# Kernel optimization log

Measured on AMD Instinct MI355X. Metric: run time of the kernel, lower is better.

## Reference

```python
import jax, jax.numpy as jnp
import numpy as np

B, S, D = 4, 2048, 1024
H = 16
HD = D // H  # head_dim = 64


def setup_inputs() -> dict:
    key = jax.random.key(0)
    ks = jax.random.split(key, 8)
    scale = 1.0 / np.sqrt(D)
    return {
        "X_Q": jax.random.normal(ks[0], (B, S, D), dtype=jnp.float32),
        "X_KV": jax.random.normal(ks[1], (B, S, D), dtype=jnp.float32),
        # q_proj: Linear(D, D), weights stored as (in, out)
        "q_w": jax.random.normal(ks[2], (D, D), dtype=jnp.float32) * scale,
        "q_b": jax.random.normal(ks[3], (D,), dtype=jnp.float32) * scale,
        # kv_proj: Linear(D, 2*D)
        "kv_w": jax.random.normal(ks[4], (D, 2 * D), dtype=jnp.float32) * scale,
        "kv_b": jax.random.normal(ks[5], (2 * D,), dtype=jnp.float32) * scale,
        # out_proj: Linear(D, D) (query_dim == input_dim)
        "out_w": jax.random.normal(ks[6], (D, D), dtype=jnp.float32) * scale,
        "out_b": jax.random.normal(ks[7], (D,), dtype=jnp.float32) * scale,
    }


def reference(X_Q, X_KV, q_w, q_b, kv_w, kv_b, out_w, out_b):
    # projections
    q = X_Q @ q_w + q_b                      # [b, s, D]
    kv = X_KV @ kv_w + kv_b                  # [b, l, 2D]
    k, v = jnp.split(kv, 2, axis=-1)         # each [b, l, D]

    def split_heads(t):
        b, m, _ = t.shape
        return t.reshape(b, m, H, HD).transpose(0, 2, 1, 3)  # [b, h, m, d]

    q, k, v = split_heads(q), split_heads(k), split_heads(v)

    # standard attention: full SxL scores (non-flash path)
    scores = jnp.einsum("bhsd,bhld->bhsl", q, k) / np.sqrt(HD)
    attn = jax.nn.softmax(scores, axis=-1)   # dropout_p = 0 -> identity
    out = jnp.einsum("bhsl,bhld->bhsd", attn, v)

    # merge heads: [b, h, s, d] -> [b, s, h*d]
    out = out.transpose(0, 2, 1, 3).reshape(B, S, D)
    return out @ out_w + out_b
```

## Files before the change

kernel.cpp:

```cpp
#include <hip/hip_runtime.h>
#include <hip/hip_bf16.h>
#include <math.h>

#define B_  4
#define S_  2048
#define D_  1024
#define H_  16
#define HD_ 64

typedef __bf16 bf16;
typedef __bf16 bf16x4 __attribute__((ext_vector_type(4)));
typedef __bf16 bf16x8 __attribute__((ext_vector_type(8)));
typedef float  floatx4 __attribute__((ext_vector_type(4)));
typedef unsigned short ushort8 __attribute__((ext_vector_type(8)));

#define QSCALE 0.18033688011112042f

__device__ __forceinline__ void async_load16(const bf16* g, bf16* l) {
  __builtin_amdgcn_global_load_lds(
      (const __attribute__((address_space(1))) void*)g,
      (__attribute__((address_space(3))) void*)l, 16, 0, 0);
}

__global__ __launch_bounds__(256) void cast_both(
    const float* __restrict__ ina, bf16* __restrict__ outa,
    const float* __restrict__ inb, bf16* __restrict__ outb) {
  int bid = blockIdx.x;
  const float* in;
  bf16* out;
  int i;
  if (bid < 8192) { in = ina; out = outa; i = (bid * 256 + threadIdx.x) * 4; }
  else            { in = inb; out = outb; i = ((bid - 8192) * 256 + threadIdx.x) * 4; }
  float4 v = *reinterpret_cast<const float4*>(in + i);
  bf16x4 o;
  o[0] = (bf16)v.x; o[1] = (bf16)v.y; o[2] = (bf16)v.z; o[3] = (bf16)v.w;
  *reinterpret_cast<bf16x4*>(out + i) = o;
}

__global__ __launch_bounds__(256) void transcast_all(
    const float* __restrict__ qw, bf16* __restrict__ qwT,
    const float* __restrict__ kvw, bf16* __restrict__ kvwT,
    const float* __restrict__ ow, bf16* __restrict__ owT) {
  __shared__ float tile[32][33];
  int bid = blockIdx.x;
  const float* in; bf16* out; int N, lb;
  if (bid < 1024)      { in = qw;  out = qwT;  N = 1024; lb = bid; }
  else if (bid < 3072) { in = kvw; out = kvwT; N = 2048; lb = bid - 1024; }
  else                 { in = ow;  out = owT;  N = 1024; lb = bid - 3072; }
  int nx = N >> 5;
  int n0 = (lb % nx) * 32, k0 = (lb / nx) * 32;
  int tx = threadIdx.x & 31, ty = threadIdx.x >> 5;
  #pragma unroll
  for (int i = ty; i < 32; i += 8)
    tile[i][tx] = in[(size_t)(k0 + i) * N + n0 + tx];
  __syncthreads();
  #pragma unroll
  for (int i = ty; i < 32; i += 8)
    out[(size_t)(n0 + i) * 1024 + k0 + tx] = (bf16)tile[tx][i];
}

template <int MODE>
__global__ __launch_bounds__(256) void gemm_bt(
    const bf16* __restrict__ A, const bf16* __restrict__ Bt,
    const float* __restrict__ bias, void* __restrict__ out,
    int M, int N, int K) {
  __shared__ bf16 As[128][64];
  __shared__ bf16 Bs[128][64];

  const int tid  = threadIdx.x;
  const int m0   = blockIdx.y * 128;
  const int n0   = blockIdx.x * 128;
  const int w    = tid >> 6;
  const int lane = tid & 63;
  const int lr   = lane & 15;
  const int lq   = lane >> 4;
  const int wm   = (w >> 1) * 64;
  const int wn   = (w & 1) * 64;

  const int srow = lane >> 3;
  const int sg   = (lane & 7) ^ srow;
  const bf16* aptr = A  + (size_t)(m0 + 32 * w + srow) * K + 8 * sg;
  const bf16* bptr = Bt + (size_t)(n0 + 32 * w + srow) * K + 8 * sg;

  floatx4 acc[4][4];
  #pragma unroll
  for (int i = 0; i < 4; i++)
    #pragma unroll
    for (int j = 0; j < 4; j++)
      acc[i][j] = floatx4{0.f, 0.f, 0.f, 0.f};

  for (int k0 = 0; k0 < K; k0 += 64) {
    __syncthreads();
    #pragma unroll
    for (int p = 0; p < 4; p++) {
      async_load16(aptr + (size_t)8 * p * K + k0, &As[32 * w + 8 * p][0]);
      async_load16(bptr + (size_t)8 * p * K + k0, &Bs[32 * w + 8 * p][0]);
    }
    __syncthreads();
    #pragma unroll
    for (int kc = 0; kc < 2; kc++) {
      const int sw = 8 * ((kc * 4 + lq) ^ (lr & 7));
      bf16x8 af[4], bfv[4];
      #pragma unroll
      for (int t = 0; t < 4; t++)
        af[t] = *reinterpret_cast<const bf16x8*>(&As[wm + 16 * t + lr][sw]);
      #pragma unroll
      for (int t = 0; t < 4; t++)
        bfv[t] = *reinterpret_cast<const bf16x8*>(&Bs[wn + 16 * t + lr][sw]);
      #pragma unroll
      for (int i = 0; i < 4; i++)
        #pragma unroll
        for (int j = 0; j < 4; j++)
          acc[i][j] = __builtin_amdgcn_mfma_f32_16x16x32_bf16(af[i], bfv[j], acc[i][j], 0, 0, 0);
    }
  }

  #pragma unroll
  for (int i = 0; i < 4; i++) {
    int row_base = m0 + wm + 16 * i + lq * 4;
    #pragma unroll
    for (int j = 0; j < 4; j++) {
      int col = n0 + wn + 16 * j + lr;
      float bv = bias[col];
      if (MODE == 2 && col >= 1024) {
        int b = row_base >> 11, s0 = row_base & 2047;
        int c = col - 1024, h = c >> 6, d = c & 63;
        bf16* Vt = (bf16*)out + (size_t)B_ * H_ * S_ * HD_;
        bf16x4 pk;
        #pragma unroll
        for (int r = 0; r < 4; r++) pk[r] = (bf16)(acc[i][j][r] + bv);
        *reinterpret_cast<bf16x4*>(
            &Vt[(((size_t)b * H_ + h) * HD_ + d) * S_ + s0]) = pk;
        continue;
      }
      #pragma unroll
      for (int r = 0; r < 4; r++) {
        int row = row_base + r;
        float v = acc[i][j][r] + bv;
        if (MODE == 0) {
          ((float*)out)[(size_t)row * N + col] = v;
        } else if (MODE == 1) {
          int b = row >> 11, s = row & 2047;
          int h = col >> 6, d = col & 63;
          ((bf16*)out)[(((size_t)b * H_ + h) * S_ + s) * HD_ + d] =
              (bf16)(v * QSCALE);
        } else {
          int b = row >> 11, s = row & 2047;
          int h = col >> 6, d = col & 63;
          ((bf16*)out)[(((size_t)b * H_ + h) * S_ + s) * HD_ + d] = (bf16)v;
        }
      }
    }
  }
}

__global__ __launch_bounds__(256, 2) void attn_kernel(
    const bf16* __restrict__ Q, const bf16* __restrict__ Kb,
    const bf16* __restrict__ Vt, bf16* __restrict__ out) {
  __shared__ bf16 smem[32768];

  const int tid  = threadIdx.x;
  const int w    = tid >> 6;
  const int lane = tid & 63;
  const int lr   = lane & 15;
  const int lq   = lane >> 4;
  const int q0   = blockIdx.x * 256;
  const int bh   = blockIdx.y;
  const size_t base = (size_t)bh * S_ * HD_;

  bf16* pw = smem + 16384 + w * 4096;

  const int srow = lane >> 3;
  const int sg   = (lane & 7) ^ srow;

  const bf16* kptr = Kb + base + (size_t)(16 * w + srow) * HD_ + 8 * sg;
  const bf16* vptr = Vt + base + (size_t)(16 * w + srow) * S_  + 8 * sg;

  #pragma unroll
  for (int p = 0; p < 2; p++) {
    async_load16(kptr + (size_t)8 * p * HD_, smem + (16 * w + 8 * p) * 64);
    async_load16(vptr + (size_t)8 * p * S_,  smem + 4096 + (16 * w + 8 * p) * 64);
  }

  bf16x8 bq[4][2];
  #pragma unroll
  for (int g = 0; g < 4; g++) {
    const bf16* qrow = Q + base + (size_t)(q0 + 64 * w + 16 * g + lr) * HD_;
    bq[g][0] = *reinterpret_cast<const bf16x8*>(qrow + lq * 8);
    bq[g][1] = *reinterpret_cast<const bf16x8*>(qrow + 32 + lq * 8);
  }

  const int sw0 = 8 * ((0 + lq) ^ (lr & 7));
  const int sw1 = 8 * ((4 + lq) ^ (lr & 7));
  const int pcolbase = 4 * (lq & 1);
  const int pswz = lr & 7;

  float l_i[4] = {0.f, 0.f, 0.f, 0.f};
  floatx4 o_acc[4][4];
  #pragma unroll
  for (int g = 0; g < 4; g++)
    #pragma unroll
    for (int t = 0; t < 4; t++) o_acc[g][t] = floatx4{0.f, 0.f, 0.f, 0.f};

  __syncthreads();

  const int NIT = S_ / 64;
  for (int it = 0; it < NIT; it++) {
    bf16* ks  = smem + (it & 1) * 8192;
    bf16* vts = ks + 4096;

    if (it + 1 < NIT) {
      bf16* ksn = smem + ((it + 1) & 1) * 8192;
      const int l0n = (it + 1) * 64;
      #pragma unroll
      for (int p = 0; p < 2; p++) {
        async_load16(kptr + (size_t)(l0n + 8 * p) * HD_, ksn + (16 * w + 8 * p) * 64);
        async_load16(vptr + (size_t)8 * p * S_ + l0n,    ksn + 4096 + (16 * w + 8 * p) * 64);
      }
    }

    #pragma unroll
    for (int t = 0; t < 4; t++) {
      bf16x8 ak0 = *reinterpret_cast<const bf16x8*>(ks + (16 * t + lr) * 64 + sw0);
      bf16x8 ak1 = *reinterpret_cast<const bf16x8*>(ks + (16 * t + lr) * 64 + sw1);
      floatx4 sc[4];
      #pragma unroll
      for (int g = 0; g < 4; g++) {
        sc[g] = __builtin_amdgcn_mfma_f32_16x16x32_bf16(ak0, bq[g][0],
                    floatx4{0.f, 0.f, 0.f, 0.f}, 0, 0, 0);
        sc[g] = __builtin_amdgcn_mfma_f32_16x16x32_bf16(ak1, bq[g][1], sc[g], 0, 0, 0);
      }
      const int pcol = 8 * ((2 * t + (lq >> 1)) ^ pswz) + pcolbase;
      #pragma unroll
      for (int g = 0; g < 4; g++) {
        bf16x4 pk;
        float lsum = 0.f;
        #pragma unroll
        for (int r = 0; r < 4; r++) {
          float p = __builtin_amdgcn_exp2f(sc[g][r]);
          lsum += p;
          pk[r] = (bf16)p;
        }
        l_i[g] += lsum;
        *reinterpret_cast<bf16x4*>(&pw[(16 * g + lr) * 64 + pcol]) = pk;
      }
    }
    __builtin_amdgcn_wave_barrier();

    #pragma unroll
    for (int kc = 0; kc < 2; kc++) {
      const int sw = kc ? sw1 : sw0;
      bf16x8 bp[4];
      #pragma unroll
      for (int g = 0; g < 4; g++)
        bp[g] = *reinterpret_cast<const bf16x8*>(&pw[(16 * g + lr) * 64 + sw]);
      #pragma unroll
      for (int t = 0; t < 4; t++) {
        bf16x8 av = *reinterpret_cast<const bf16x8*>(vts + (16 * t + lr) * 64 + sw);
        #pragma unroll
        for (int g = 0; g < 4; g++)
          o_acc[g][t] = __builtin_amdgcn_mfma_f32_16x16x32_bf16(av, bp[g], o_acc[g][t], 0, 0, 0);
      }
    }

    __syncthreads();
  }

  #pragma unroll
  for (int g = 0; g < 4; g++) {
    l_i[g] += __shfl_xor(l_i[g], 16, 64);
    l_i[g] += __shfl_xor(l_i[g], 32, 64);
  }

  const int b = bh >> 4, h = bh & 15;
  #pragma unroll
  for (int g = 0; g < 4; g++) {
    const float inv = 1.0f / l_i[g];
    const int qrow = q0 + 64 * w + 16 * g + lr;
    bf16* orow = out + ((size_t)b * S_ + qrow) * D_ + h * HD_;
    #pragma unroll
    for (int t = 0; t < 4; t++) {
      bf16x4 pk;
      #pragma unroll
      for (int r = 0; r < 4; r++) pk[r] = (bf16)(o_acc[g][t][r] * inv);
      *reinterpret_cast<bf16x4*>(&orow[16 * t + lq * 4]) = pk;
    }
  }
}

extern "C" void kernel_launch(void* const* d_in, const int* in_sizes, int n_in,
                              void* d_out, int out_size, void* d_ws, size_t ws_size,
                              hipStream_t stream) {
  const float* X_Q   = (const float*)d_in[0];
  const float* X_KV  = (const float*)d_in[1];
  const float* q_w   = (const float*)d_in[2];
  const float* q_b   = (const float*)d_in[3];
  const float* kv_w  = (const float*)d_in[4];
  const float* kv_b  = (const float*)d_in[5];
  const float* out_w = (const float*)d_in[6];
  const float* out_b = (const float*)d_in[7];
  float* out = (float*)d_out;

  char* ws = (char*)d_ws;
  const size_t MB = 1024 * 1024;
  bf16* Xq   = (bf16*)(ws + 0);
  bf16* Xkv  = (bf16*)(ws + 16 * MB);
  bf16* Qb   = (bf16*)(ws + 32 * MB);
  bf16* Kb   = (bf16*)(ws + 48 * MB);
  bf16* qwT  = (bf16*)(ws + 80 * MB);
  bf16* kvwT = (bf16*)(ws + 82 * MB);
  bf16* owT  = (bf16*)(ws + 86 * MB);
  bf16* Vt   = Kb + (size_t)B_ * H_ * S_ * HD_;
  bf16* attn = Xq;

  cast_both<<<16384, 256, 0, stream>>>(X_Q, Xq, X_KV, Xkv);
  transcast_all<<<4096, 256, 0, stream>>>(q_w, qwT, kv_w, kvwT, out_w, owT);

  gemm_bt<1><<<dim3(8, 64), 256, 0, stream>>>(Xq, qwT, q_b, Qb, 8192, 1024, 1024);
  gemm_bt<2><<<dim3(16, 64), 256, 0, stream>>>(Xkv, kvwT, kv_b, Kb, 8192, 2048, 1024);
  attn_kernel<<<dim3(8, 64), 256, 0, stream>>>(Qb, Kb, Vt, attn);
  gemm_bt<0><<<dim3(8, 64), 256, 0, stream>>>(attn, owT, out_b, out, 8192, 1024, 1024);
}
```

Measured before the change: 323.4 us.

## Keep softmax probabilities in registers via bpermute and halve attention query tile

```diff
diff --git a/kernel.cpp b/kernel.cpp
--- a/kernel.cpp
+++ b/kernel.cpp
@@ -20,6 +20,12 @@
   __builtin_amdgcn_global_load_lds(
       (const __attribute__((address_space(1))) void*)g,
       (__attribute__((address_space(3))) void*)l, 16, 0, 0);
+}
+
+__device__ __forceinline__ unsigned packbf2(float a, float b) {
+  union { bf16 h[2]; unsigned u; } x;
+  x.h[0] = (bf16)a; x.h[1] = (bf16)b;
+  return x.u;
 }
 
 __global__ __launch_bounds__(256) void cast_both(
@@ -154,21 +160,19 @@
   }
 }
 
-__global__ __launch_bounds__(256, 2) void attn_kernel(
+__global__ __launch_bounds__(256, 4) void attn_kernel(
     const bf16* __restrict__ Q, const bf16* __restrict__ Kb,
     const bf16* __restrict__ Vt, bf16* __restrict__ out) {
-  __shared__ bf16 smem[32768];
+  __shared__ bf16 smem[16384];
 
   const int tid  = threadIdx.x;
   const int w    = tid >> 6;
   const int lane = tid & 63;
   const int lr   = lane & 15;
   const int lq   = lane >> 4;
-  const int q0   = blockIdx.x * 256;
+  const int q0   = blockIdx.x * 128;
   const int bh   = blockIdx.y;
   const size_t base = (size_t)bh * S_ * HD_;
-
-  bf16* pw = smem + 16384 + w * 4096;
 
   const int srow = lane >> 3;
   const int sg   = (lane & 7) ^ srow;
@@ -182,23 +186,23 @@
     async_load16(vptr + (size_t)8 * p * S_,  smem + 4096 + (16 * w + 8 * p) * 64);
   }
 
-  bf16x8 bq[4][2];
-  #pragma unroll
-  for (int g = 0; g < 4; g++) {
-    const bf16* qrow = Q + base + (size_t)(q0 + 64 * w + 16 * g + lr) * HD_;
+  bf16x8 bq[2][2];
+  #pragma unroll
+  for (int g = 0; g < 2; g++) {
+    const bf16* qrow = Q + base + (size_t)(q0 + 32 * w + 16 * g + lr) * HD_;
     bq[g][0] = *reinterpret_cast<const bf16x8*>(qrow + lq * 8);
     bq[g][1] = *reinterpret_cast<const bf16x8*>(qrow + 32 + lq * 8);
   }
 
   const int sw0 = 8 * ((0 + lq) ^ (lr & 7));
   const int sw1 = 8 * ((4 + lq) ^ (lr & 7));
-  const int pcolbase = 4 * (lq & 1);
-  const int pswz = lr & 7;
-
-  float l_i[4] = {0.f, 0.f, 0.f, 0.f};
-  floatx4 o_acc[4][4];
-  #pragma unroll
-  for (int g = 0; g < 4; g++)
+  const int idxU = ((lq & 1) * 32 + lr) * 4;
+  const int idxW = idxU + 64;
+
+  float l_i[2] = {0.f, 0.f};
+  floatx4 o_acc[2][4];
+  #pragma unroll
+  for (int g = 0; g < 2; g++)
     #pragma unroll
     for (int t = 0; t < 4; t++) o_acc[g][t] = floatx4{0.f, 0.f, 0.f, 0.f};
 
@@ -220,46 +224,52 @@
     }
 
     #pragma unroll
-    for (int t = 0; t < 4; t++) {
-      bf16x8 ak0 = *reinterpret_cast<const bf16x8*>(ks + (16 * t + lr) * 64 + sw0);
-      bf16x8 ak1 = *reinterpret_cast<const bf16x8*>(ks + (16 * t + lr) * 64 + sw1);
-      floatx4 sc[4];
-      #pragma unroll
-      for (int g = 0; g < 4; g++) {
-        sc[g] = __builtin_amdgcn_mfma_f32_16x16x32_bf16(ak0, bq[g][0],
-                    floatx4{0.f, 0.f, 0.f, 0.f}, 0, 0, 0);
-        sc[g] = __builtin_amdgcn_mfma_f32_16x16x32_bf16(ak1, bq[g][1], sc[g], 0, 0, 0);
-      }
-      const int pcol = 8 * ((2 * t + (lq >> 1)) ^ pswz) + pcolbase;
-      #pragma unroll
-      for (int g = 0; g < 4; g++) {
-        bf16x4 pk;
-        float lsum = 0.f;
-        #pragma unroll
-        for (int r = 0; r < 4; r++) {
-          float p = __builtin_amdgcn_exp2f(sc[g][r]);
-          lsum += p;
-          pk[r] = (bf16)p;
+    for (int th = 0; th < 2; th++) {
+      unsigned cg[2][2][2];
+      #pragma unroll
+      for (int tt = 0; tt < 2; tt++) {
+        const int t = 2 * th + tt;
+        bf16x8 ak0 = *reinterpret_cast<const bf16x8*>(ks + (16 * t + lr) * 64 + sw0);
+        bf16x8 ak1 = *reinterpret_cast<const bf16x8*>(ks + (16 * t + lr) * 64 + sw1);
+        #pragma unroll
+        for (int g = 0; g < 2; g++) {
+          floatx4 sc = __builtin_amdgcn_mfma_f32_16x16x32_bf16(
+              ak0, bq[g][0], floatx4{0.f, 0.f, 0.f, 0.f}, 0, 0, 0);
+          sc = __builtin_amdgcn_mfma_f32_16x16x32_bf16(ak1, bq[g][1], sc, 0, 0, 0);
+          float p0 = __builtin_amdgcn_exp2f(sc[0]);
+          float p1 = __builtin_amdgcn_exp2f(sc[1]);
+          float p2 = __builtin_amdgcn_exp2f(sc[2]);
+          float p3 = __builtin_amdgcn_exp2f(sc[3]);
+          l_i[g] += (p0 + p1) + (p2 + p3);
+          cg[g][tt][0] = packbf2(p0, p1);
+          cg[g][tt][1] = packbf2(p2, p3);
         }
-        l_i[g] += lsum;
-        *reinterpret_cast<bf16x4*>(&pw[(16 * g + lr) * 64 + pcol]) = pk;
-      }
-    }
-    __builtin_amdgcn_wave_barrier();
-
-    #pragma unroll
-    for (int kc = 0; kc < 2; kc++) {
-      const int sw = kc ? sw1 : sw0;
-      bf16x8 bp[4];
-      #pragma unroll
-      for (int g = 0; g < 4; g++)
-        bp[g] = *reinterpret_cast<const bf16x8*>(&pw[(16 * g + lr) * 64 + sw]);
-      #pragma unroll
-      for (int t = 0; t < 4; t++) {
-        bf16x8 av = *reinterpret_cast<const bf16x8*>(vts + (16 * t + lr) * 64 + sw);
-        #pragma unroll
-        for (int g = 0; g < 4; g++)
-          o_acc[g][t] = __builtin_amdgcn_mfma_f32_16x16x32_bf16(av, bp[g], o_acc[g][t], 0, 0, 0);
+      }
+
+      bf16x8 bp[2];
+      #pragma unroll
+      for (int g = 0; g < 2; g++) {
+        union { unsigned u[4]; bf16x8 v; } f;
+        #pragma unroll
+        for (int d = 0; d < 2; d++) {
+          int X = (int)cg[g][0][d], Y = (int)cg[g][1][d];
+          unsigned Ux = (unsigned)__builtin_amdgcn_ds_bpermute(idxU, X);
+          unsigned Uy = (unsigned)__builtin_amdgcn_ds_bpermute(idxU, Y);
+          unsigned Wx = (unsigned)__builtin_amdgcn_ds_bpermute(idxW, X);
+          unsigned Wy = (unsigned)__builtin_amdgcn_ds_bpermute(idxW, Y);
+          f.u[d]     = (lq < 2) ? Ux : Uy;
+          f.u[2 + d] = (lq < 2) ? Wx : Wy;
+        }
+        bp[g] = f.v;
+      }
+
+      const int sw = th ? sw1 : sw0;
+      #pragma unroll
+      for (int t2 = 0; t2 < 4; t2++) {
+        bf16x8 av = *reinterpret_cast<const bf16x8*>(vts + (16 * t2 + lr) * 64 + sw);
+        #pragma unroll
+        for (int g = 0; g < 2; g++)
+          o_acc[g][t2] = __builtin_amdgcn_mfma_f32_16x16x32_bf16(av, bp[g], o_acc[g][t2], 0, 0, 0);
       }
     }
 
@@ -267,16 +277,16 @@
   }
 
   #pragma unroll
-  for (int g = 0; g < 4; g++) {
+  for (int g = 0; g < 2; g++) {
     l_i[g] += __shfl_xor(l_i[g], 16, 64);
     l_i[g] += __shfl_xor(l_i[g], 32, 64);
   }
 
   const int b = bh >> 4, h = bh & 15;
   #pragma unroll
-  for (int g = 0; g < 4; g++) {
+  for (int g = 0; g < 2; g++) {
     const float inv = 1.0f / l_i[g];
-    const int qrow = q0 + 64 * w + 16 * g + lr;
+    const int qrow = q0 + 32 * w + 16 * g + lr;
     bf16* orow = out + ((size_t)b * S_ + qrow) * D_ + h * HD_;
     #pragma unroll
     for (int t = 0; t < 4; t++) {
@@ -318,6 +328,6 @@
 
   gemm_bt<1><<<dim3(8, 64), 256, 0, stream>>>(Xq, qwT, q_b, Qb, 8192, 1024, 1024);
   gemm_bt<2><<<dim3(16, 64), 256, 0, stream>>>(Xkv, kvwT, kv_b, Kb, 8192, 2048, 1024);
-  attn_kernel<<<dim3(8, 64), 256, 0, stream>>>(Qb, Kb, Vt, attn);
+  attn_kernel<<<dim3(16, 64), 256, 0, stream>>>(Qb, Kb, Vt, attn);
   gemm_bt<0><<<dim3(8, 64), 256, 0, stream>>>(attn, owT, out_b, out, 8192, 1024, 1024);
 }
```

Result: slower. 349.9 us (+8.2%).

## Interleave QK^T and PV MFMA phases in attention loop and reorder grid

Applied to the files above, without the earlier changes.

```diff
diff --git a/kernel.cpp b/kernel.cpp
--- a/kernel.cpp
+++ b/kernel.cpp
@@ -164,8 +164,8 @@
   const int lane = tid & 63;
   const int lr   = lane & 15;
   const int lq   = lane >> 4;
-  const int q0   = blockIdx.x * 256;
-  const int bh   = blockIdx.y;
+  const int bh   = blockIdx.x;
+  const int q0   = blockIdx.y * 256;
   const size_t base = (size_t)bh * S_ * HD_;
 
   bf16* pw = smem + 16384 + w * 4096;
@@ -219,8 +219,7 @@
       }
     }
 
-    #pragma unroll
-    for (int t = 0; t < 4; t++) {
+    auto qkt = [&](int t) {
       bf16x8 ak0 = *reinterpret_cast<const bf16x8*>(ks + (16 * t + lr) * 64 + sw0);
       bf16x8 ak1 = *reinterpret_cast<const bf16x8*>(ks + (16 * t + lr) * 64 + sw1);
       floatx4 sc[4];
@@ -244,22 +243,46 @@
         l_i[g] += lsum;
         *reinterpret_cast<bf16x4*>(&pw[(16 * g + lr) * 64 + pcol]) = pk;
       }
-    }
+    };
+
+    qkt(0);
+    qkt(1);
     __builtin_amdgcn_wave_barrier();
 
-    #pragma unroll
-    for (int kc = 0; kc < 2; kc++) {
-      const int sw = kc ? sw1 : sw0;
-      bf16x8 bp[4];
+    {
+      bf16x8 bp0[4], av0[4];
       #pragma unroll
       for (int g = 0; g < 4; g++)
-        bp[g] = *reinterpret_cast<const bf16x8*>(&pw[(16 * g + lr) * 64 + sw]);
-      #pragma unroll
-      for (int t = 0; t < 4; t++) {
-        bf16x8 av = *reinterpret_cast<const bf16x8*>(vts + (16 * t + lr) * 64 + sw);
+        bp0[g] = *reinterpret_cast<const bf16x8*>(&pw[(16 * g + lr) * 64 + sw0]);
+      #pragma unroll
+      for (int t2 = 0; t2 < 4; t2++)
+        av0[t2] = *reinterpret_cast<const bf16x8*>(vts + (16 * t2 + lr) * 64 + sw0);
+      qkt(2);
+      #pragma unroll
+      for (int t2 = 0; t2 < 2; t2++)
         #pragma unroll
         for (int g = 0; g < 4; g++)
-          o_acc[g][t] = __builtin_amdgcn_mfma_f32_16x16x32_bf16(av, bp[g], o_acc[g][t], 0, 0, 0);
+          o_acc[g][t2] = __builtin_amdgcn_mfma_f32_16x16x32_bf16(av0[t2], bp0[g], o_acc[g][t2], 0, 0, 0);
+      qkt(3);
+      #pragma unroll
+      for (int t2 = 2; t2 < 4; t2++)
+        #pragma unroll
+        for (int g = 0; g < 4; g++)
+          o_acc[g][t2] = __builtin_amdgcn_mfma_f32_16x16x32_bf16(av0[t2], bp0[g], o_acc[g][t2], 0, 0, 0);
+    }
+    __builtin_amdgcn_wave_barrier();
+
+    {
+      bf16x8 bp1[4];
+      #pragma unroll
+      for (int g = 0; g < 4; g++)
+        bp1[g] = *reinterpret_cast<const bf16x8*>(&pw[(16 * g + lr) * 64 + sw1]);
+      #pragma unroll
+      for (int t2 = 0; t2 < 4; t2++) {
+        bf16x8 av = *reinterpret_cast<const bf16x8*>(vts + (16 * t2 + lr) * 64 + sw1);
+        #pragma unroll
+        for (int g = 0; g < 4; g++)
+          o_acc[g][t2] = __builtin_amdgcn_mfma_f32_16x16x32_bf16(av, bp1[g], o_acc[g][t2], 0, 0, 0);
       }
     }
 
@@ -318,6 +341,6 @@
 
   gemm_bt<1><<<dim3(8, 64), 256, 0, stream>>>(Xq, qwT, q_b, Qb, 8192, 1024, 1024);
   gemm_bt<2><<<dim3(16, 64), 256, 0, stream>>>(Xkv, kvwT, kv_b, Kb, 8192, 2048, 1024);
-  attn_kernel<<<dim3(8, 64), 256, 0, stream>>>(Qb, Kb, Vt, attn);
+  attn_kernel<<<dim3(64, 8), 256, 0, stream>>>(Qb, Kb, Vt, attn);
   gemm_bt<0><<<dim3(8, 64), 256, 0, stream>>>(attn, owT, out_b, out, 8192, 1024, 1024);
 }
```

New measurement: 308.5 us. 4.6% less time.
